# Kernel optimization log

Hardware: AMD Instinct MI355X
Metric: run time of the kernel (lower is better)

Reference implementation:

```python
import jax, jax.numpy as jnp
import numpy as np

B, S, E, H = 1, 8192, 1024, 16
D = E // H
SEG_LENS = [2048, 4096, 8192]
DILATIONS = [1, 2, 4]


def setup_inputs() -> dict:
    key = jax.random.key(0)
    k0, k1, k2 = jax.random.split(key, 3)
    sc_in = 1.0 / np.sqrt(E)
    return {
        "x": jax.random.normal(k0, (B, S, E), jnp.float32),
        "w_qkv": jax.random.normal(k1, (3 * E, E), jnp.float32) * sc_in,
        "b_qkv": jnp.zeros((3 * E,), jnp.float32),
        "w_out": jax.random.normal(k2, (E, E), jnp.float32) * sc_in,
        "b_out": jnp.zeros((E,), jnp.float32),
    }


def _sdpa(q, k, v):
    # q,k,v: [B,H,N,D]; standard scaled dot-product attention (non-causal)
    scale = 1.0 / np.sqrt(q.shape[-1])
    scores = jnp.einsum('bhqd,bhkd->bhqk', q, k) * scale
    probs = jax.nn.softmax(scores, axis=-1)
    return jnp.einsum('bhqk,bhkd->bhqd', probs, v)


def reference(x, w_qkv, b_qkv, w_out, b_out):
    # QKV projection: torch Linear is x @ W^T + b
    qkv = x @ w_qkv.T + b_qkv                       # [B,S,3E]
    qkv = qkv.reshape(B, S, 3, H, D).transpose(2, 0, 3, 1, 4)  # [3,B,H,S,D]
    q, k, v = qkv[0], qkv[1], qkv[2]

    seg_outputs = []
    for seg_len, dil in zip(SEG_LENS, DILATIONS):
        if seg_len > S:
            continue
        if dil > 1:
            n = min(seg_len, S // dil)
            pos = np.arange(0, n * dil, dil)        # strided dilated gather
        else:
            pos = np.arange(seg_len)                # leading segment
        o = _sdpa(q[:, :, pos], k[:, :, pos], v[:, :, pos])
        # scatter back to full length (zero elsewhere); also handles zero-padding
        full = jnp.zeros((B, H, S, D), x.dtype).at[:, :, pos, :].set(o)
        seg_outputs.append(full)

    if len(seg_outputs) == 0:
        out = jnp.zeros((B, H, S, D), x.dtype)
    else:
        out = seg_outputs[0]
        for so in seg_outputs[1:]:
            out = out + so
        out = out / len(seg_outputs)                # stack(...).mean(0)

    out = out.transpose(0, 2, 1, 3).reshape(B, S, E)
    return out @ w_out.T + b_out
```

## Files before the change

### kernel.cpp

```cpp
#include <hip/hip_runtime.h>


typedef __attribute__((ext_vector_type(8))) short bf16x8;
typedef __attribute__((ext_vector_type(4))) float f32x4;

#define MFMA(a, b, c) __builtin_amdgcn_mfma_f32_16x16x32_bf16((a), (b), (c), 0, 0, 0)

#if __has_builtin(__builtin_amdgcn_exp2f)
#define EXP2(x) __builtin_amdgcn_exp2f(x)
#else
#define EXP2(x) exp2f(x)
#endif

static __device__ __forceinline__ unsigned short f2bf(float f) {
  unsigned int u = __float_as_uint(f);
  unsigned int r = (u + 0x7FFFu + ((u >> 16) & 1u)) >> 16;
  return (unsigned short)r;
}

__global__ void cvt_all(const float* __restrict__ x, const float* __restrict__ wq,
                        const float* __restrict__ wo,
                        unsigned short* __restrict__ xb,
                        unsigned short* __restrict__ wqb,
                        unsigned short* __restrict__ wob) {
  int i = blockIdx.x * 256 + threadIdx.x;
  const float* src;
  unsigned short* dst;
  if (i < 1048576) { src = x; dst = xb; }
  else if (i < 1441792) { src = wq + (size_t)(i - 1048576) * 8 - 0; dst = wqb; i -= 1048576; src = wq; }
  else { i -= 1441792; src = wo; dst = wob; }
  const float4* p = (const float4*)src + (size_t)i * 2;
  float4 a = p[0];
  float4 b = p[1];
  union { bf16x8 v; unsigned short u[8]; } o;
  o.u[0] = f2bf(a.x); o.u[1] = f2bf(a.y); o.u[2] = f2bf(a.z); o.u[3] = f2bf(a.w);
  o.u[4] = f2bf(b.x); o.u[5] = f2bf(b.y); o.u[6] = f2bf(b.z); o.u[7] = f2bf(b.w);
  *((bf16x8*)dst + i) = o.v;
}

template <int EPILOGUE>
__global__ __launch_bounds__(256, 2) void gemm_bt(
    const unsigned short* __restrict__ A, const unsigned short* __restrict__ B,
    const float* __restrict__ bias, void* __restrict__ Cout, int N, int K) {
  __shared__ unsigned short At[128 * 32];
  __shared__ unsigned short Bt[128 * 32];
  const int tid = threadIdx.x;
  const int wave = tid >> 6, lane = tid & 63;
  const int quad = lane >> 4, lc = lane & 15;
  const int wm = (wave >> 1) * 64, wn = (wave & 1) * 64;
  const int m0 = blockIdx.x * 128, n0 = blockIdx.y * 128;

  f32x4 acc[4][4] = {};

  for (int k0 = 0; k0 < K; k0 += 32) {
    __syncthreads();
#pragma unroll
    for (int issue = 0; issue < 2; ++issue) {
      const int cbase = issue * 256 + wave * 64;
      const int c = cbase + lane;
      const int row = c >> 2, col8 = (c & 3) * 8;
      __builtin_amdgcn_global_load_lds(
          (const __attribute__((address_space(1))) void*)&A[(size_t)(m0 + row) * K + k0 + col8],
          (__attribute__((address_space(3))) void*)&At[cbase * 8], 16, 0, 0);
      __builtin_amdgcn_global_load_lds(
          (const __attribute__((address_space(1))) void*)&B[(size_t)(n0 + row) * K + k0 + col8],
          (__attribute__((address_space(3))) void*)&Bt[cbase * 8], 16, 0, 0);
    }
    __syncthreads();
    bf16x8 af[4], bfr[4];
#pragma unroll
    for (int t = 0; t < 4; ++t)
      af[t] = *(const bf16x8*)&At[(wm + t * 16 + lc) * 32 + quad * 8];
#pragma unroll
    for (int t = 0; t < 4; ++t)
      bfr[t] = *(const bf16x8*)&Bt[(wn + t * 16 + lc) * 32 + quad * 8];
#pragma unroll
    for (int i = 0; i < 4; ++i)
#pragma unroll
      for (int j = 0; j < 4; ++j)
        acc[i][j] = MFMA(bfr[j], af[i], acc[i][j]);
  }

#pragma unroll
  for (int j = 0; j < 4; ++j) {
    const int nc0 = n0 + wn + j * 16 + quad * 4;
    const float4 bs4 = *(const float4*)&bias[nc0];
    if (EPILOGUE == 0) {
      const int which = nc0 >> 10, rem = nc0 & 1023;
      const int hh = rem >> 6, d0 = rem & 63;
      const float sc = (which == 0) ? 0.18033688f : 1.0f;
      unsigned short* base =
          (unsigned short*)Cout + ((size_t)(which * 16 + hh)) * 8192 * 64 + d0;
#pragma unroll
      for (int i = 0; i < 4; ++i) {
        const int grow = m0 + wm + i * 16 + lc;
        const unsigned int p0 = __float_as_uint((acc[i][j][0] + bs4.x) * sc) + 0x8000u;
        const unsigned int p1 = __float_as_uint((acc[i][j][1] + bs4.y) * sc) + 0x8000u;
        const unsigned int p2 = __float_as_uint((acc[i][j][2] + bs4.z) * sc) + 0x8000u;
        const unsigned int p3 = __float_as_uint((acc[i][j][3] + bs4.w) * sc) + 0x8000u;
        uint2 w;
        w.x = __builtin_amdgcn_perm(p1, p0, 0x07060302u);
        w.y = __builtin_amdgcn_perm(p3, p2, 0x07060302u);
        *(uint2*)(base + (size_t)grow * 64) = w;
      }
    } else {
      float* op = (float*)Cout;
#pragma unroll
      for (int i = 0; i < 4; ++i) {
        const int grow = m0 + wm + i * 16 + lc;
        float4 v;
        v.x = acc[i][j][0] + bs4.x;
        v.y = acc[i][j][1] + bs4.y;
        v.z = acc[i][j][2] + bs4.z;
        v.w = acc[i][j][3] + bs4.w;
        *(float4*)&op[(size_t)grow * N + nc0] = v;
      }
    }
  }
}

__global__ void transpose_v(const unsigned short* __restrict__ v,
                            unsigned short* __restrict__ vt1,
                            unsigned short* __restrict__ vt2,
                            unsigned short* __restrict__ vt3) {
  __shared__ unsigned short Tt[64 * 72];
  const int tid = threadIdx.x;
  const int h = blockIdx.y;
  const int bx = blockIdx.x;
  const unsigned short* src = v + (size_t)h * 8192 * 64;
  unsigned short* dst;
  int dil, Nk, t0;
  if (bx < 32)      { dst = vt1; dil = 1; Nk = 2048; t0 = bx; }
  else if (bx < 96) { dst = vt2; dil = 2; Nk = 4096; t0 = bx - 32; }
  else              { dst = vt3; dil = 4; Nk = 2048; t0 = bx - 96; }
  dst += (size_t)h * 64 * Nk;
  const int j0 = t0 * 64;
#pragma unroll
  for (int it = 0; it < 2; ++it) {
    const int slot = tid + it * 256;
    const int jj = slot >> 3, c8 = (slot & 7) * 8;
    *(bf16x8*)&Tt[jj * 72 + c8] =
        *(const bf16x8*)&src[(size_t)(j0 + jj) * dil * 64 + c8];
  }
  __syncthreads();
  const int d = tid >> 2, pg = (tid & 3) * 16;
  union { bf16x8 v2[2]; unsigned short u[16]; } ob;
#pragma unroll
  for (int t = 0; t < 16; ++t) {
    const int pos = pg + t;
    const int w = pos & 31;
    const int jj = (pos & 32) | (((w >> 2) & 1) * 16 + (w >> 3) * 4 + (w & 3));
    ob.u[t] = Tt[jj * 72 + d];
  }
  *(bf16x8*)&dst[(size_t)d * Nk + j0 + pg] = ob.v2[0];
  *(bf16x8*)&dst[(size_t)d * Nk + j0 + pg + 8] = ob.v2[1];
}

__global__ __launch_bounds__(256, 3) void flash_all(
    const unsigned short* __restrict__ qkvb,
    const unsigned short* __restrict__ vt1, float* __restrict__ o1,
    const unsigned short* __restrict__ vt2, float* __restrict__ o2a,
    float* __restrict__ o2b, float* __restrict__ l2a, float* __restrict__ l2b,
    const unsigned short* __restrict__ vt3, float* __restrict__ o3) {
  __shared__ unsigned short Smem[2][2 * 64 * 64];

  const int bx = blockIdx.x;
  const int x = bx & 7, g = bx >> 3;
  const int h = x + ((g >= 48) ? 8 : 0);
  const int gg = (g >= 48) ? g - 48 : g;
  int z, qt, kb0;
  const unsigned short* vt;
  float* o;
  float* lout = nullptr;
  bool split = false;
  if (gg < 32) {
    z = 1; qt = gg >> 1; kb0 = (gg & 1) * 2048; split = true;
    vt = vt2; o = (gg & 1) ? o2b : o2a; lout = (gg & 1) ? l2b : l2a;
  } else if (gg < 40) {
    z = 0; qt = gg - 32; kb0 = 0; vt = vt1; o = o1;
  } else {
    z = 2; qt = gg - 40; kb0 = 0; vt = vt3; o = o3;
  }
  const int Nk = (z == 1) ? 4096 : 2048;
  const int kbEnd = kb0 + 2048;
  const int dil = 1 << z;

  const int tid = threadIdx.x;
  const int wave = tid >> 6, lane = tid & 63;
  const int quad = lane >> 4, lc = lane & 15;

  const unsigned short* qh = qkvb + (size_t)h * 8192 * 64;
  const unsigned short* kh = qkvb + (size_t)(16 + h) * 8192 * 64;
  const unsigned short* vh = vt + (size_t)h * 64 * Nk;

  bf16x8 qf[4][2];
#pragma unroll
  for (int mb = 0; mb < 4; ++mb) {
    const size_t qrow = (size_t)(qt * 256 + wave * 64 + mb * 16 + lc) * dil;
    qf[mb][0] = *(const bf16x8*)&qh[qrow * 64 + quad * 8];
    qf[mb][1] = *(const bf16x8*)&qh[qrow * 64 + quad * 8 + 32];
  }

  union { bf16x8 v; unsigned short u[8]; } one_u;
#pragma unroll
  for (int t = 0; t < 8; ++t) one_u.u[t] = 0x3F80;
  const bf16x8 vone = one_u.v;

  f32x4 oacc[4][4] = {};
  f32x4 lacc[4] = {};

  const int srow = tid >> 3, scol = tid & 7;
  const int swz = (scol ^ (srow & 7)) * 8;

  bf16x8 kg0 = *(const bf16x8*)&kh[(size_t)((kb0 + srow) * dil) * 64 + scol * 8];
  bf16x8 kg1 = *(const bf16x8*)&kh[(size_t)((kb0 + srow + 32) * dil) * 64 + scol * 8];
  bf16x8 vg0 = *(const bf16x8*)&vh[(size_t)srow * Nk + kb0 + scol * 8];
  bf16x8 vg1 = *(const bf16x8*)&vh[(size_t)(srow + 32) * Nk + kb0 + scol * 8];
  *(bf16x8*)&Smem[0][srow * 64 + swz] = kg0;
  *(bf16x8*)&Smem[0][(srow + 32) * 64 + swz] = kg1;
  *(bf16x8*)&Smem[0][4096 + srow * 64 + swz] = vg0;
  *(bf16x8*)&Smem[0][4096 + (srow + 32) * 64 + swz] = vg1;
  __syncthreads();

  int p = 0;
  for (int kb = kb0; kb < kbEnd; kb += 64) {
    const bool more = (kb + 64 < kbEnd);
    if (more) {
      const int nk = kb + 64;
      kg0 = *(const bf16x8*)&kh[(size_t)((nk + srow) * dil) * 64 + scol * 8];
      kg1 = *(const bf16x8*)&kh[(size_t)((nk + srow + 32) * dil) * 64 + scol * 8];
      vg0 = *(const bf16x8*)&vh[(size_t)srow * Nk + nk + scol * 8];
      vg1 = *(const bf16x8*)&vh[(size_t)(srow + 32) * Nk + nk + scol * 8];
    }
    const unsigned short* Kt = Smem[p];
    const unsigned short* Vt = Smem[p] + 4096;

#pragma unroll
    for (int ks = 0; ks < 2; ++ks) {
      f32x4 st[2][4];
#pragma unroll
      for (int t = 0; t < 2; ++t) {
        const int row = (ks * 2 + t) * 16 + lc;
        const bf16x8 ka0 = *(const bf16x8*)&Kt[row * 64 + ((quad ^ (lc & 7)) * 8)];
        const bf16x8 ka1 = *(const bf16x8*)&Kt[row * 64 + (((4 + quad) ^ (lc & 7)) * 8)];
#pragma unroll
        for (int mb = 0; mb < 4; ++mb) {
          f32x4 zz = {};
          zz = MFMA(ka0, qf[mb][0], zz);
          st[t][mb] = MFMA(ka1, qf[mb][1], zz);
        }
      }

      bf16x8 pb[4];
#pragma unroll
      for (int mb = 0; mb < 4; ++mb) {
        union { bf16x8 v; unsigned int u[4]; } pu;
#pragma unroll
        for (int t = 0; t < 2; ++t) {
          const unsigned int a0 = __float_as_uint(EXP2(st[t][mb][0]));
          const unsigned int a1 = __float_as_uint(EXP2(st[t][mb][1]));
          const unsigned int a2 = __float_as_uint(EXP2(st[t][mb][2]));
          const unsigned int a3 = __float_as_uint(EXP2(st[t][mb][3]));
          pu.u[t * 2 + 0] = __builtin_amdgcn_perm(a1, a0, 0x07060302u);
          pu.u[t * 2 + 1] = __builtin_amdgcn_perm(a3, a2, 0x07060302u);
        }
        pb[mb] = pu.v;
      }

#pragma unroll
      for (int nb = 0; nb < 4; ++nb) {
        const int vrow = nb * 16 + lc;
        const bf16x8 va = *(const bf16x8*)&Vt[vrow * 64 + (((ks * 4 + quad) ^ (lc & 7)) * 8)];
#pragma unroll
        for (int mb = 0; mb < 4; ++mb)
          oacc[mb][nb] = MFMA(va, pb[mb], oacc[mb][nb]);
      }
#pragma unroll
      for (int mb = 0; mb < 4; ++mb) lacc[mb] = MFMA(vone, pb[mb], lacc[mb]);
    }

    if (more) {
      *(bf16x8*)&Smem[p ^ 1][srow * 64 + swz] = kg0;
      *(bf16x8*)&Smem[p ^ 1][(srow + 32) * 64 + swz] = kg1;
      *(bf16x8*)&Smem[p ^ 1][4096 + srow * 64 + swz] = vg0;
      *(bf16x8*)&Smem[p ^ 1][4096 + (srow + 32) * 64 + swz] = vg1;
    }
    __syncthreads();
    p ^= 1;
  }

  float* W = (float*)Smem + wave * 16 * 64;
  const int g2 = lane >> 2, s4 = lane & 3;
#pragma unroll
  for (int mb = 0; mb < 4; ++mb) {
    const float inv = split ? 1.0f : 1.0f / (3.0f * lacc[mb][0]);
    if (split && quad == 0)
      lout[(size_t)h * 4096 + qt * 256 + wave * 64 + mb * 16 + lc] = lacc[mb][0];
#pragma unroll
    for (int nb = 0; nb < 4; ++nb) {
      const int c = nb * 4 + quad;
      const int cs = (c & 8) | ((c & 7) ^ (lc & 7));
      f32x4 val = oacc[mb][nb];
      val *= inv;
      *(f32x4*)&W[lc * 64 + cs * 4] = val;
    }
    const size_t base = (size_t)(qt * 256 + wave * 64 + mb * 16 + g2) * 1024 +
                        (size_t)h * 64 + s4 * 16;
#pragma unroll
    for (int c2 = 0; c2 < 4; ++c2) {
      const int c = s4 * 4 + c2;
      const int cs = (c & 8) | ((c & 7) ^ (g2 & 7));
      *(float4*)&o[base + c2 * 4] = *(const float4*)&W[g2 * 64 + cs * 4];
    }
  }
}

__global__ void combine(const float* __restrict__ o1,
                        const float* __restrict__ o2a, const float* __restrict__ o2b,
                        const float* __restrict__ l2a, const float* __restrict__ l2b,
                        const float* __restrict__ o3,
                        unsigned short* __restrict__ a3b) {
  const int idx = blockIdx.x * 256 + threadIdx.x;
  const int s = idx >> 7, e = (idx & 127) * 8;
  float acc[8] = {};
  if (s < 2048) {
    const float* p = &o1[(size_t)s * 1024 + e];
#pragma unroll
    for (int t = 0; t < 8; ++t) acc[t] += p[t];
  }
  if (!(s & 1)) {
    const int j = s >> 1, hh = e >> 6;
    const float la = l2a[(size_t)hh * 4096 + j];
    const float lb = l2b[(size_t)hh * 4096 + j];
    const float w = 1.0f / (3.0f * (la + lb));
    const float* pa = &o2a[(size_t)j * 1024 + e];
    const float* pb = &o2b[(size_t)j * 1024 + e];
#pragma unroll
    for (int t = 0; t < 8; ++t) acc[t] += (pa[t] + pb[t]) * w;
  }
  if (!(s & 3)) {
    const float* p = &o3[(size_t)(s >> 2) * 1024 + e];
#pragma unroll
    for (int t = 0; t < 8; ++t) acc[t] += p[t];
  }
  union { bf16x8 v; unsigned short u[8]; } ob;
#pragma unroll
  for (int t = 0; t < 8; ++t) ob.u[t] = f2bf(acc[t]);
  *(bf16x8*)&a3b[(size_t)s * 1024 + e] = ob.v;
}

extern "C" void kernel_launch(void* const* d_in, const int* in_sizes, int n_in,
                              void* d_out, int out_size, void* d_ws, size_t ws_size,
                              hipStream_t stream) {
  const float* x     = (const float*)d_in[0];
  const float* w_qkv = (const float*)d_in[1];
  const float* b_qkv = (const float*)d_in[2];
  const float* w_out = (const float*)d_in[3];
  const float* b_out = (const float*)d_in[4];
  float* out = (float*)d_out;

  char* ws = (char*)d_ws;
  unsigned short* qkvb  = (unsigned short*)(ws);
  float*          o1    = (float*)(ws + 33554432);
  float*          o3    = (float*)(ws + 41943040);
  unsigned short* vt1   = (unsigned short*)(ws + 50331648);
  unsigned short* vt2   = (unsigned short*)(ws + 54525952);
  unsigned short* vt3   = (unsigned short*)(ws + 62914560);
  float*          o2a   = (float*)(ws + 67108864);
  unsigned short* wqkvb = (unsigned short*)(ws + 83886080);
  float*          l2a   = (float*)(ws + 83886080);
  float*          l2b   = (float*)(ws + 84148224);
  unsigned short* woutb = (unsigned short*)(ws + 90177536);
  unsigned short* xb    = (unsigned short*)(ws + 92274688);
  float*          o2b   = (float*)(ws + 92274688);
  unsigned short* a3b   = (unsigned short*)(ws + 50331648);

  cvt_all<<<dim3(6144), dim3(256), 0, stream>>>(x, w_qkv, w_out, xb, wqkvb, woutb);

  gemm_bt<0><<<dim3(64, 24), dim3(256), 0, stream>>>(xb, wqkvb, b_qkv, qkvb, 3072, 1024);

  transpose_v<<<dim3(128, 16), dim3(256), 0, stream>>>(qkvb + (size_t)32 * 8192 * 64,
                                                       vt1, vt2, vt3);

  flash_all<<<dim3(768), dim3(256), 0, stream>>>(qkvb, vt1, o1, vt2, o2a, o2b,
                                                 l2a, l2b, vt3, o3);

  combine<<<dim3(4096), dim3(256), 0, stream>>>(o1, o2a, o2b, l2a, l2b, o3, a3b);

  gemm_bt<1><<<dim3(64, 8), dim3(256), 0, stream>>>(a3b, woutb, b_out, out, 1024, 1024);
}
```

Before: 341.1 us.

## Split attention keys across waves within a block and reduce via LDS atomics

Each flash block now handles 64 queries, and its four waves each process a quarter of the key range using private LDS tiles with no block-wide barriers in the main loop. Partial outputs and row sums are merged through shared-memory float atomics before normalization. This removes the separate split-K halves and the l2 buffers for segment two, and raises the grid from 768 to 2048 blocks. The cost is Q fragments reloaded per wave, more LDS atomic traffic in the epilogue, and smaller 32-key steps per iteration.

```diff
diff --git a/kernel.cpp b/kernel.cpp
--- a/kernel.cpp
+++ b/kernel.cpp
@@ -27,7 +27,7 @@
   const float* src;
   unsigned short* dst;
   if (i < 1048576) { src = x; dst = xb; }
-  else if (i < 1441792) { src = wq + (size_t)(i - 1048576) * 8 - 0; dst = wqb; i -= 1048576; src = wq; }
+  else if (i < 1441792) { i -= 1048576; src = wq; dst = wqb; }
   else { i -= 1441792; src = wo; dst = wob; }
   const float4* p = (const float4*)src + (size_t)i * 2;
   float4 a = p[0];
@@ -159,30 +159,21 @@
 __global__ __launch_bounds__(256, 3) void flash_all(
     const unsigned short* __restrict__ qkvb,
     const unsigned short* __restrict__ vt1, float* __restrict__ o1,
-    const unsigned short* __restrict__ vt2, float* __restrict__ o2a,
-    float* __restrict__ o2b, float* __restrict__ l2a, float* __restrict__ l2b,
+    const unsigned short* __restrict__ vt2, float* __restrict__ o2,
     const unsigned short* __restrict__ vt3, float* __restrict__ o3) {
-  __shared__ unsigned short Smem[2][2 * 64 * 64];
+  __shared__ unsigned short Smem[4 * 4096];
 
   const int bx = blockIdx.x;
-  const int x = bx & 7, g = bx >> 3;
-  const int h = x + ((g >= 48) ? 8 : 0);
-  const int gg = (g >= 48) ? g - 48 : g;
-  int z, qt, kb0;
+  const int x = bx & 7, r2 = bx >> 3;
+  const int h = (r2 & 1) * 8 + x;
+  const int unit = r2 >> 1;
+  int z, qt;
   const unsigned short* vt;
   float* o;
-  float* lout = nullptr;
-  bool split = false;
-  if (gg < 32) {
-    z = 1; qt = gg >> 1; kb0 = (gg & 1) * 2048; split = true;
-    vt = vt2; o = (gg & 1) ? o2b : o2a; lout = (gg & 1) ? l2b : l2a;
-  } else if (gg < 40) {
-    z = 0; qt = gg - 32; kb0 = 0; vt = vt1; o = o1;
-  } else {
-    z = 2; qt = gg - 40; kb0 = 0; vt = vt3; o = o3;
-  }
+  if (unit < 64)      { z = 1; qt = unit;      vt = vt2; o = o2; }
+  else if (unit < 96) { z = 0; qt = unit - 64; vt = vt1; o = o1; }
+  else                { z = 2; qt = unit - 96; vt = vt3; o = o3; }
   const int Nk = (z == 1) ? 4096 : 2048;
-  const int kbEnd = kb0 + 2048;
   const int dil = 1 << z;
 
   const int tid = threadIdx.x;
@@ -193,10 +184,13 @@
   const unsigned short* kh = qkvb + (size_t)(16 + h) * 8192 * 64;
   const unsigned short* vh = vt + (size_t)h * 64 * Nk;
 
+  unsigned short* Kt = Smem + wave * 4096;
+  unsigned short* Vt = Kt + 2048;
+
   bf16x8 qf[4][2];
 #pragma unroll
   for (int mb = 0; mb < 4; ++mb) {
-    const size_t qrow = (size_t)(qt * 256 + wave * 64 + mb * 16 + lc) * dil;
+    const size_t qrow = (size_t)(qt * 64 + mb * 16 + lc) * dil;
     qf[mb][0] = *(const bf16x8*)&qh[qrow * 64 + quad * 8];
     qf[mb][1] = *(const bf16x8*)&qh[qrow * 64 + quad * 8 + 32];
   }
@@ -209,115 +203,118 @@
   f32x4 oacc[4][4] = {};
   f32x4 lacc[4] = {};
 
-  const int srow = tid >> 3, scol = tid & 7;
-  const int swz = (scol ^ (srow & 7)) * 8;
-
-  bf16x8 kg0 = *(const bf16x8*)&kh[(size_t)((kb0 + srow) * dil) * 64 + scol * 8];
-  bf16x8 kg1 = *(const bf16x8*)&kh[(size_t)((kb0 + srow + 32) * dil) * 64 + scol * 8];
-  bf16x8 vg0 = *(const bf16x8*)&vh[(size_t)srow * Nk + kb0 + scol * 8];
-  bf16x8 vg1 = *(const bf16x8*)&vh[(size_t)(srow + 32) * Nk + kb0 + scol * 8];
-  *(bf16x8*)&Smem[0][srow * 64 + swz] = kg0;
-  *(bf16x8*)&Smem[0][(srow + 32) * 64 + swz] = kg1;
-  *(bf16x8*)&Smem[0][4096 + srow * 64 + swz] = vg0;
-  *(bf16x8*)&Smem[0][4096 + (srow + 32) * 64 + swz] = vg1;
+  const int c0 = wave * (Nk >> 2);
+  const int cLen = Nk >> 2;
+
+  const int krow = lane >> 3, kch = lane & 7;
+  const int vdr = lane >> 2, vch = lane & 3;
+  const int kswz = (kch ^ (krow & 7)) * 8;
+  const int vswz = (vch ^ (vdr & 3)) * 8;
+
+  bf16x8 kg[4], vg[4];
+#pragma unroll
+  for (int i = 0; i < 4; ++i) {
+    kg[i] = *(const bf16x8*)&kh[(size_t)((c0 + i * 8 + krow) * dil) * 64 + kch * 8];
+    vg[i] = *(const bf16x8*)&vh[(size_t)(i * 16 + vdr) * Nk + c0 + vch * 8];
+  }
+#pragma unroll
+  for (int i = 0; i < 4; ++i) {
+    *(bf16x8*)&Kt[(i * 8 + krow) * 64 + kswz] = kg[i];
+    *(bf16x8*)&Vt[(i * 16 + vdr) * 32 + vswz] = vg[i];
+  }
+
+  for (int kb = 0; kb < cLen; kb += 32) {
+    const bool more = (kb + 32 < cLen);
+    if (more) {
+      const int nk = c0 + kb + 32;
+#pragma unroll
+      for (int i = 0; i < 4; ++i) {
+        kg[i] = *(const bf16x8*)&kh[(size_t)((nk + i * 8 + krow) * dil) * 64 + kch * 8];
+        vg[i] = *(const bf16x8*)&vh[(size_t)(i * 16 + vdr) * Nk + nk + vch * 8];
+      }
+    }
+
+    f32x4 st[2][4];
+#pragma unroll
+    for (int t = 0; t < 2; ++t) {
+      const int row = t * 16 + lc;
+      const bf16x8 ka0 = *(const bf16x8*)&Kt[row * 64 + ((quad ^ (lc & 7)) * 8)];
+      const bf16x8 ka1 = *(const bf16x8*)&Kt[row * 64 + (((4 + quad) ^ (lc & 7)) * 8)];
+#pragma unroll
+      for (int mb = 0; mb < 4; ++mb) {
+        f32x4 zz = {};
+        zz = MFMA(ka0, qf[mb][0], zz);
+        st[t][mb] = MFMA(ka1, qf[mb][1], zz);
+      }
+    }
+
+    bf16x8 pb[4];
+#pragma unroll
+    for (int mb = 0; mb < 4; ++mb) {
+      union { bf16x8 v; unsigned int u[4]; } pu;
+#pragma unroll
+      for (int t = 0; t < 2; ++t) {
+        const unsigned int a0 = __float_as_uint(EXP2(st[t][mb][0]));
+        const unsigned int a1 = __float_as_uint(EXP2(st[t][mb][1]));
+        const unsigned int a2 = __float_as_uint(EXP2(st[t][mb][2]));
+        const unsigned int a3 = __float_as_uint(EXP2(st[t][mb][3]));
+        pu.u[t * 2 + 0] = __builtin_amdgcn_perm(a1, a0, 0x07060302u);
+        pu.u[t * 2 + 1] = __builtin_amdgcn_perm(a3, a2, 0x07060302u);
+      }
+      pb[mb] = pu.v;
+    }
+
+#pragma unroll
+    for (int nb = 0; nb < 4; ++nb) {
+      const bf16x8 va = *(const bf16x8*)&Vt[(nb * 16 + lc) * 32 + ((quad ^ (lc & 3)) * 8)];
+#pragma unroll
+      for (int mb = 0; mb < 4; ++mb)
+        oacc[mb][nb] = MFMA(va, pb[mb], oacc[mb][nb]);
+    }
+#pragma unroll
+    for (int mb = 0; mb < 4; ++mb) lacc[mb] = MFMA(vone, pb[mb], lacc[mb]);
+
+    if (more) {
+      __builtin_amdgcn_s_waitcnt(0xC07F);
+#pragma unroll
+      for (int i = 0; i < 4; ++i) {
+        *(bf16x8*)&Kt[(i * 8 + krow) * 64 + kswz] = kg[i];
+        *(bf16x8*)&Vt[(i * 16 + vdr) * 32 + vswz] = vg[i];
+      }
+    }
+  }
+
   __syncthreads();
-
-  int p = 0;
-  for (int kb = kb0; kb < kbEnd; kb += 64) {
-    const bool more = (kb + 64 < kbEnd);
-    if (more) {
-      const int nk = kb + 64;
-      kg0 = *(const bf16x8*)&kh[(size_t)((nk + srow) * dil) * 64 + scol * 8];
-      kg1 = *(const bf16x8*)&kh[(size_t)((nk + srow + 32) * dil) * 64 + scol * 8];
-      vg0 = *(const bf16x8*)&vh[(size_t)srow * Nk + nk + scol * 8];
-      vg1 = *(const bf16x8*)&vh[(size_t)(srow + 32) * Nk + nk + scol * 8];
-    }
-    const unsigned short* Kt = Smem[p];
-    const unsigned short* Vt = Smem[p] + 4096;
-
-#pragma unroll
-    for (int ks = 0; ks < 2; ++ks) {
-      f32x4 st[2][4];
-#pragma unroll
-      for (int t = 0; t < 2; ++t) {
-        const int row = (ks * 2 + t) * 16 + lc;
-        const bf16x8 ka0 = *(const bf16x8*)&Kt[row * 64 + ((quad ^ (lc & 7)) * 8)];
-        const bf16x8 ka1 = *(const bf16x8*)&Kt[row * 64 + (((4 + quad) ^ (lc & 7)) * 8)];
-#pragma unroll
-        for (int mb = 0; mb < 4; ++mb) {
-          f32x4 zz = {};
-          zz = MFMA(ka0, qf[mb][0], zz);
-          st[t][mb] = MFMA(ka1, qf[mb][1], zz);
-        }
-      }
-
-      bf16x8 pb[4];
-#pragma unroll
-      for (int mb = 0; mb < 4; ++mb) {
-        union { bf16x8 v; unsigned int u[4]; } pu;
-#pragma unroll
-        for (int t = 0; t < 2; ++t) {
-          const unsigned int a0 = __float_as_uint(EXP2(st[t][mb][0]));
-          const unsigned int a1 = __float_as_uint(EXP2(st[t][mb][1]));
-          const unsigned int a2 = __float_as_uint(EXP2(st[t][mb][2]));
-          const unsigned int a3 = __float_as_uint(EXP2(st[t][mb][3]));
-          pu.u[t * 2 + 0] = __builtin_amdgcn_perm(a1, a0, 0x07060302u);
-          pu.u[t * 2 + 1] = __builtin_amdgcn_perm(a3, a2, 0x07060302u);
-        }
-        pb[mb] = pu.v;
-      }
-
-#pragma unroll
-      for (int nb = 0; nb < 4; ++nb) {
-        const int vrow = nb * 16 + lc;
-        const bf16x8 va = *(const bf16x8*)&Vt[vrow * 64 + (((ks * 4 + quad) ^ (lc & 7)) * 8)];
-#pragma unroll
-        for (int mb = 0; mb < 4; ++mb)
-          oacc[mb][nb] = MFMA(va, pb[mb], oacc[mb][nb]);
-      }
-#pragma unroll
-      for (int mb = 0; mb < 4; ++mb) lacc[mb] = MFMA(vone, pb[mb], lacc[mb]);
-    }
-
-    if (more) {
-      *(bf16x8*)&Smem[p ^ 1][srow * 64 + swz] = kg0;
-      *(bf16x8*)&Smem[p ^ 1][(srow + 32) * 64 + swz] = kg1;
-      *(bf16x8*)&Smem[p ^ 1][4096 + srow * 64 + swz] = vg0;
-      *(bf16x8*)&Smem[p ^ 1][4096 + (srow + 32) * 64 + swz] = vg1;
-    }
-    __syncthreads();
-    p ^= 1;
-  }
-
-  float* W = (float*)Smem + wave * 16 * 64;
-  const int g2 = lane >> 2, s4 = lane & 3;
+  float* Wm = (float*)Smem;
+  float* Wl = (float*)Smem + 4096;
+  for (int t = tid; t < 4160; t += 256) ((float*)Smem)[t] = 0.0f;
+  __syncthreads();
 #pragma unroll
   for (int mb = 0; mb < 4; ++mb) {
-    const float inv = split ? 1.0f : 1.0f / (3.0f * lacc[mb][0]);
-    if (split && quad == 0)
-      lout[(size_t)h * 4096 + qt * 256 + wave * 64 + mb * 16 + lc] = lacc[mb][0];
-#pragma unroll
-    for (int nb = 0; nb < 4; ++nb) {
-      const int c = nb * 4 + quad;
-      const int cs = (c & 8) | ((c & 7) ^ (lc & 7));
-      f32x4 val = oacc[mb][nb];
-      val *= inv;
-      *(f32x4*)&W[lc * 64 + cs * 4] = val;
-    }
-    const size_t base = (size_t)(qt * 256 + wave * 64 + mb * 16 + g2) * 1024 +
-                        (size_t)h * 64 + s4 * 16;
-#pragma unroll
-    for (int c2 = 0; c2 < 4; ++c2) {
-      const int c = s4 * 4 + c2;
-      const int cs = (c & 8) | ((c & 7) ^ (g2 & 7));
-      *(float4*)&o[base + c2 * 4] = *(const float4*)&W[g2 * 64 + cs * 4];
-    }
-  }
-}
-
-__global__ void combine(const float* __restrict__ o1,
-                        const float* __restrict__ o2a, const float* __restrict__ o2b,
-                        const float* __restrict__ l2a, const float* __restrict__ l2b,
+#pragma unroll
+    for (int nb = 0; nb < 4; ++nb)
+#pragma unroll
+      for (int r = 0; r < 4; ++r)
+        atomicAdd(&Wm[(nb * 16 + quad * 4 + r) * 64 + mb * 16 + lc], oacc[mb][nb][r]);
+    if (quad == 0) atomicAdd(&Wl[mb * 16 + lc], lacc[mb][0]);
+  }
+  __syncthreads();
+
+  const int q = tid >> 2, dg = tid & 3;
+  const float inv = 1.0f / (3.0f * Wl[q]);
+  const size_t base = (size_t)(qt * 64 + q) * 1024 + (size_t)h * 64 + dg * 16;
+#pragma unroll
+  for (int c2 = 0; c2 < 4; ++c2) {
+    float4 v;
+    v.x = Wm[(dg * 16 + c2 * 4 + 0) * 64 + q] * inv;
+    v.y = Wm[(dg * 16 + c2 * 4 + 1) * 64 + q] * inv;
+    v.z = Wm[(dg * 16 + c2 * 4 + 2) * 64 + q] * inv;
+    v.w = Wm[(dg * 16 + c2 * 4 + 3) * 64 + q] * inv;
+    *(float4*)&o[base + c2 * 4] = v;
+  }
+}
+
+__global__ void combine(const float* __restrict__ o1, const float* __restrict__ o2,
                         const float* __restrict__ o3,
                         unsigned short* __restrict__ a3b) {
   const int idx = blockIdx.x * 256 + threadIdx.x;
@@ -329,14 +326,9 @@
     for (int t = 0; t < 8; ++t) acc[t] += p[t];
   }
   if (!(s & 1)) {
-    const int j = s >> 1, hh = e >> 6;
-    const float la = l2a[(size_t)hh * 4096 + j];
-    const float lb = l2b[(size_t)hh * 4096 + j];
-    const float w = 1.0f / (3.0f * (la + lb));
-    const float* pa = &o2a[(size_t)j * 1024 + e];
-    const float* pb = &o2b[(size_t)j * 1024 + e];
-#pragma unroll
-    for (int t = 0; t < 8; ++t) acc[t] += (pa[t] + pb[t]) * w;
+    const float* p = &o2[(size_t)(s >> 1) * 1024 + e];
+#pragma unroll
+    for (int t = 0; t < 8; ++t) acc[t] += p[t];
   }
   if (!(s & 3)) {
     const float* p = &o3[(size_t)(s >> 2) * 1024 + e];
@@ -366,13 +358,10 @@
   unsigned short* vt1   = (unsigned short*)(ws + 50331648);
   unsigned short* vt2   = (unsigned short*)(ws + 54525952);
   unsigned short* vt3   = (unsigned short*)(ws + 62914560);
-  float*          o2a   = (float*)(ws + 67108864);
+  float*          o2    = (float*)(ws + 67108864);
   unsigned short* wqkvb = (unsigned short*)(ws + 83886080);
-  float*          l2a   = (float*)(ws + 83886080);
-  float*          l2b   = (float*)(ws + 84148224);
   unsigned short* woutb = (unsigned short*)(ws + 90177536);
   unsigned short* xb    = (unsigned short*)(ws + 92274688);
-  float*          o2b   = (float*)(ws + 92274688);
   unsigned short* a3b   = (unsigned short*)(ws + 50331648);
 
   cvt_all<<<dim3(6144), dim3(256), 0, stream>>>(x, w_qkv, w_out, xb, wqkvb, woutb);
@@ -382,10 +371,9 @@
   transpose_v<<<dim3(128, 16), dim3(256), 0, stream>>>(qkvb + (size_t)32 * 8192 * 64,
                                                        vt1, vt2, vt3);
 
-  flash_all<<<dim3(768), dim3(256), 0, stream>>>(qkvb, vt1, o1, vt2, o2a, o2b,
-                                                 l2a, l2b, vt3, o3);
-
-  combine<<<dim3(4096), dim3(256), 0, stream>>>(o1, o2a, o2b, l2a, l2b, o3, a3b);
+  flash_all<<<dim3(2048), dim3(256), 0, stream>>>(qkvb, vt1, o1, vt2, o2, vt3, o3);
+
+  combine<<<dim3(4096), dim3(256), 0, stream>>>(o1, o2, o3, a3b);
 
   gemm_bt<1><<<dim3(64, 8), dim3(256), 0, stream>>>(a3b, woutb, b_out, out, 1024, 1024);
 }
```

After: 780.9 us. 2.29x slower.

## Split all attention segments along keys and store partial outputs as bf16

Applied to the files above, without the earlier changes.

Every dilated segment, not only the middle one, is now split into two key halves, giving 1024 uniform work units of equal length instead of 768 uneven ones. Partial outputs are written as bf16 with row sums, and the combine kernel merges them. Launch bounds are raised to 4 blocks per SM. The aim is better load balance and less intermediate memory traffic, at the cost of extra partial buffers, an extra bf16 rounding step before merging, and possible register pressure from the higher occupancy target.

```diff
diff --git a/kernel.cpp b/kernel.cpp
--- a/kernel.cpp
+++ b/kernel.cpp
@@ -27,7 +27,7 @@
   const float* src;
   unsigned short* dst;
   if (i < 1048576) { src = x; dst = xb; }
-  else if (i < 1441792) { src = wq + (size_t)(i - 1048576) * 8 - 0; dst = wqb; i -= 1048576; src = wq; }
+  else if (i < 1441792) { i -= 1048576; src = wq; dst = wqb; }
   else { i -= 1441792; src = wo; dst = wob; }
   const float4* p = (const float4*)src + (size_t)i * 2;
   float4 a = p[0];
@@ -156,34 +156,34 @@
   *(bf16x8*)&dst[(size_t)d * Nk + j0 + pg + 8] = ob.v2[1];
 }
 
-__global__ __launch_bounds__(256, 3) void flash_all(
+__global__ __launch_bounds__(256, 4) void flash_all(
     const unsigned short* __restrict__ qkvb,
-    const unsigned short* __restrict__ vt1, float* __restrict__ o1,
-    const unsigned short* __restrict__ vt2, float* __restrict__ o2a,
-    float* __restrict__ o2b, float* __restrict__ l2a, float* __restrict__ l2b,
-    const unsigned short* __restrict__ vt3, float* __restrict__ o3) {
+    const unsigned short* __restrict__ vt1, unsigned short* __restrict__ o1a,
+    unsigned short* __restrict__ o1b, float* __restrict__ l1a, float* __restrict__ l1b,
+    const unsigned short* __restrict__ vt2, unsigned short* __restrict__ o2a,
+    unsigned short* __restrict__ o2b, float* __restrict__ l2a, float* __restrict__ l2b,
+    const unsigned short* __restrict__ vt3, unsigned short* __restrict__ o3a,
+    unsigned short* __restrict__ o3b, float* __restrict__ l3a, float* __restrict__ l3b) {
   __shared__ unsigned short Smem[2][2 * 64 * 64];
 
   const int bx = blockIdx.x;
-  const int x = bx & 7, g = bx >> 3;
-  const int h = x + ((g >= 48) ? 8 : 0);
-  const int gg = (g >= 48) ? g - 48 : g;
-  int z, qt, kb0;
-  const unsigned short* vt;
-  float* o;
-  float* lout = nullptr;
-  bool split = false;
-  if (gg < 32) {
-    z = 1; qt = gg >> 1; kb0 = (gg & 1) * 2048; split = true;
-    vt = vt2; o = (gg & 1) ? o2b : o2a; lout = (gg & 1) ? l2b : l2a;
-  } else if (gg < 40) {
-    z = 0; qt = gg - 32; kb0 = 0; vt = vt1; o = o1;
-  } else {
-    z = 2; qt = gg - 40; kb0 = 0; vt = vt3; o = o3;
-  }
+  const int x = bx & 7, u = bx >> 3;
+  const int h = (u & 1) * 8 + x;
+  const int unit = u >> 1;
+  int z, qt;
+  if (unit < 32)      { z = 1; qt = unit >> 1; }
+  else if (unit < 48) { z = 0; qt = (unit - 32) >> 1; }
+  else                { z = 2; qt = (unit - 48) >> 1; }
+  const int kc = unit & 1;
   const int Nk = (z == 1) ? 4096 : 2048;
-  const int kbEnd = kb0 + 2048;
+  const int half = Nk >> 1;
+  const int kb0 = kc * half, kbEnd = kb0 + half;
   const int dil = 1 << z;
+  const unsigned short* vt = (z == 0) ? vt1 : (z == 1) ? vt2 : vt3;
+  unsigned short* o = (z == 0) ? (kc ? o1b : o1a)
+                    : (z == 1) ? (kc ? o2b : o2a) : (kc ? o3b : o3a);
+  float* lout = (z == 0) ? (kc ? l1b : l1a)
+              : (z == 1) ? (kc ? l2b : l2a) : (kc ? l3b : l3a);
 
   const int tid = threadIdx.x;
   const int wave = tid >> 6, lane = tid & 63;
@@ -293,55 +293,73 @@
   const int g2 = lane >> 2, s4 = lane & 3;
 #pragma unroll
   for (int mb = 0; mb < 4; ++mb) {
-    const float inv = split ? 1.0f : 1.0f / (3.0f * lacc[mb][0]);
-    if (split && quad == 0)
-      lout[(size_t)h * 4096 + qt * 256 + wave * 64 + mb * 16 + lc] = lacc[mb][0];
+    if (quad == 0)
+      lout[(size_t)h * Nk + qt * 256 + wave * 64 + mb * 16 + lc] = lacc[mb][0];
 #pragma unroll
     for (int nb = 0; nb < 4; ++nb) {
       const int c = nb * 4 + quad;
       const int cs = (c & 8) | ((c & 7) ^ (lc & 7));
-      f32x4 val = oacc[mb][nb];
-      val *= inv;
-      *(f32x4*)&W[lc * 64 + cs * 4] = val;
+      *(f32x4*)&W[lc * 64 + cs * 4] = oacc[mb][nb];
     }
     const size_t base = (size_t)(qt * 256 + wave * 64 + mb * 16 + g2) * 1024 +
                         (size_t)h * 64 + s4 * 16;
+    float vals[16];
 #pragma unroll
     for (int c2 = 0; c2 < 4; ++c2) {
       const int c = s4 * 4 + c2;
       const int cs = (c & 8) | ((c & 7) ^ (g2 & 7));
-      *(float4*)&o[base + c2 * 4] = *(const float4*)&W[g2 * 64 + cs * 4];
-    }
-  }
-}
-
-__global__ void combine(const float* __restrict__ o1,
-                        const float* __restrict__ o2a, const float* __restrict__ o2b,
-                        const float* __restrict__ l2a, const float* __restrict__ l2b,
-                        const float* __restrict__ o3,
-                        unsigned short* __restrict__ a3b) {
+      const float4 v = *(const float4*)&W[g2 * 64 + cs * 4];
+      vals[c2 * 4 + 0] = v.x; vals[c2 * 4 + 1] = v.y;
+      vals[c2 * 4 + 2] = v.z; vals[c2 * 4 + 3] = v.w;
+    }
+    union { bf16x8 v; unsigned short u2[8]; } ob0, ob1;
+#pragma unroll
+    for (int t = 0; t < 8; ++t) { ob0.u2[t] = f2bf(vals[t]); ob1.u2[t] = f2bf(vals[8 + t]); }
+    *(bf16x8*)&o[base] = ob0.v;
+    *(bf16x8*)&o[base + 8] = ob1.v;
+  }
+}
+
+static __device__ __forceinline__ float bf2f(unsigned short u) {
+  return __uint_as_float((unsigned int)u << 16);
+}
+__global__ void combine(
+    const unsigned short* __restrict__ o1a, const unsigned short* __restrict__ o1b,
+    const float* __restrict__ l1a, const float* __restrict__ l1b,
+    const unsigned short* __restrict__ o2a, const unsigned short* __restrict__ o2b,
+    const float* __restrict__ l2a, const float* __restrict__ l2b,
+    const unsigned short* __restrict__ o3a, const unsigned short* __restrict__ o3b,
+    const float* __restrict__ l3a, const float* __restrict__ l3b,
+    unsigned short* __restrict__ a3b) {
   const int idx = blockIdx.x * 256 + threadIdx.x;
   const int s = idx >> 7, e = (idx & 127) * 8;
+  const int hh = e >> 6;
   float acc[8] = {};
   if (s < 2048) {
-    const float* p = &o1[(size_t)s * 1024 + e];
-#pragma unroll
-    for (int t = 0; t < 8; ++t) acc[t] += p[t];
+    const float w = 1.0f / (3.0f * (l1a[(size_t)hh * 2048 + s] + l1b[(size_t)hh * 2048 + s]));
+    union { bf16x8 v; unsigned short u[8]; } pa, pb;
+    pa.v = *(const bf16x8*)&o1a[(size_t)s * 1024 + e];
+    pb.v = *(const bf16x8*)&o1b[(size_t)s * 1024 + e];
+#pragma unroll
+    for (int t = 0; t < 8; ++t) acc[t] += (bf2f(pa.u[t]) + bf2f(pb.u[t])) * w;
   }
   if (!(s & 1)) {
-    const int j = s >> 1, hh = e >> 6;
-    const float la = l2a[(size_t)hh * 4096 + j];
-    const float lb = l2b[(size_t)hh * 4096 + j];
-    const float w = 1.0f / (3.0f * (la + lb));
-    const float* pa = &o2a[(size_t)j * 1024 + e];
-    const float* pb = &o2b[(size_t)j * 1024 + e];
-#pragma unroll
-    for (int t = 0; t < 8; ++t) acc[t] += (pa[t] + pb[t]) * w;
+    const int j = s >> 1;
+    const float w = 1.0f / (3.0f * (l2a[(size_t)hh * 4096 + j] + l2b[(size_t)hh * 4096 + j]));
+    union { bf16x8 v; unsigned short u[8]; } pa, pb;
+    pa.v = *(const bf16x8*)&o2a[(size_t)j * 1024 + e];
+    pb.v = *(const bf16x8*)&o2b[(size_t)j * 1024 + e];
+#pragma unroll
+    for (int t = 0; t < 8; ++t) acc[t] += (bf2f(pa.u[t]) + bf2f(pb.u[t])) * w;
   }
   if (!(s & 3)) {
-    const float* p = &o3[(size_t)(s >> 2) * 1024 + e];
-#pragma unroll
-    for (int t = 0; t < 8; ++t) acc[t] += p[t];
+    const int j = s >> 2;
+    const float w = 1.0f / (3.0f * (l3a[(size_t)hh * 2048 + j] + l3b[(size_t)hh * 2048 + j]));
+    union { bf16x8 v; unsigned short u[8]; } pa, pb;
+    pa.v = *(const bf16x8*)&o3a[(size_t)j * 1024 + e];
+    pb.v = *(const bf16x8*)&o3b[(size_t)j * 1024 + e];
+#pragma unroll
+    for (int t = 0; t < 8; ++t) acc[t] += (bf2f(pa.u[t]) + bf2f(pb.u[t])) * w;
   }
   union { bf16x8 v; unsigned short u[8]; } ob;
 #pragma unroll
@@ -361,18 +379,24 @@
 
   char* ws = (char*)d_ws;
   unsigned short* qkvb  = (unsigned short*)(ws);
-  float*          o1    = (float*)(ws + 33554432);
-  float*          o3    = (float*)(ws + 41943040);
+  unsigned short* o1a   = (unsigned short*)(ws + 33554432);
+  unsigned short* o1b   = (unsigned short*)(ws + 37748736);
+  unsigned short* o3a   = (unsigned short*)(ws + 41943040);
+  unsigned short* o3b   = (unsigned short*)(ws + 46137344);
   unsigned short* vt1   = (unsigned short*)(ws + 50331648);
   unsigned short* vt2   = (unsigned short*)(ws + 54525952);
   unsigned short* vt3   = (unsigned short*)(ws + 62914560);
-  float*          o2a   = (float*)(ws + 67108864);
+  unsigned short* o2a   = (unsigned short*)(ws + 67108864);
+  unsigned short* o2b   = (unsigned short*)(ws + 75497472);
   unsigned short* wqkvb = (unsigned short*)(ws + 83886080);
   float*          l2a   = (float*)(ws + 83886080);
   float*          l2b   = (float*)(ws + 84148224);
+  float*          l1a   = (float*)(ws + 84410368);
+  float*          l1b   = (float*)(ws + 84541440);
+  float*          l3a   = (float*)(ws + 84672512);
+  float*          l3b   = (float*)(ws + 84803584);
   unsigned short* woutb = (unsigned short*)(ws + 90177536);
   unsigned short* xb    = (unsigned short*)(ws + 92274688);
-  float*          o2b   = (float*)(ws + 92274688);
   unsigned short* a3b   = (unsigned short*)(ws + 50331648);
 
   cvt_all<<<dim3(6144), dim3(256), 0, stream>>>(x, w_qkv, w_out, xb, wqkvb, woutb);
@@ -382,10 +406,12 @@
   transpose_v<<<dim3(128, 16), dim3(256), 0, stream>>>(qkvb + (size_t)32 * 8192 * 64,
                                                        vt1, vt2, vt3);
 
-  flash_all<<<dim3(768), dim3(256), 0, stream>>>(qkvb, vt1, o1, vt2, o2a, o2b,
-                                                 l2a, l2b, vt3, o3);
-
-  combine<<<dim3(4096), dim3(256), 0, stream>>>(o1, o2a, o2b, l2a, l2b, o3, a3b);
+  flash_all<<<dim3(1024), dim3(256), 0, stream>>>(
+      qkvb, vt1, o1a, o1b, l1a, l1b, vt2, o2a, o2b, l2a, l2b,
+      vt3, o3a, o3b, l3a, l3b);
+
+  combine<<<dim3(4096), dim3(256), 0, stream>>>(
+      o1a, o1b, l1a, l1b, o2a, o2b, l2a, l2b, o3a, o3b, l3a, l3b, a3b);
 
   gemm_bt<1><<<dim3(64, 8), dim3(256), 0, stream>>>(a3b, woutb, b_out, out, 1024, 1024);
 }
```

New measurement: 944.0 us. 177% more time.
